# Kernel tuning notes

Measured on AMD Instinct MI355X. Metric: run time of the kernel, lower is better.

Reference implementation:

```python
import jax, jax.numpy as jnp
import numpy as np

B, N, D, H, DK, DV, HID = 4, 16384, 512, 8, 64, 64, 2048
LN_EPS = 1e-5   # torch nn.LayerNorm default
ATTN_EPS = 1e-6 # eps passed to LinearMultiHeadAttention


def _ln(h, g, b):
    m = jnp.mean(h, axis=-1, keepdims=True)
    v = jnp.mean(jnp.square(h - m), axis=-1, keepdims=True)
    return (h - m) * jax.lax.rsqrt(v + LN_EPS) * g + b


def setup_inputs() -> dict:
    key = jax.random.key(0)
    ks = jax.random.split(key, 8)
    w = lambda k, *sh: (jax.random.normal(k, sh, jnp.float32) * 0.02)
    return {
        "x": jax.random.normal(ks[0], (B, N, D), jnp.float32),
        "ln1_g": jnp.ones((D,), jnp.float32), "ln1_b": jnp.zeros((D,), jnp.float32),
        "Wq": w(ks[1], D, H * DK), "bq": jnp.zeros((H * DK,), jnp.float32),
        "Wk": w(ks[2], D, H * DK), "bk": jnp.zeros((H * DK,), jnp.float32),
        "Wv": w(ks[3], D, H * DV), "bv": jnp.zeros((H * DV,), jnp.float32),
        "Wo": w(ks[4], H * DV, D), "bo": jnp.zeros((D,), jnp.float32),
        "ln2_g": jnp.ones((D,), jnp.float32), "ln2_b": jnp.zeros((D,), jnp.float32),
        "W1": w(ks[5], D, HID), "b1": jnp.zeros((HID,), jnp.float32),
        "W2": w(ks[6], HID, D), "b2": jnp.zeros((D,), jnp.float32),
    }


def reference(x, ln1_g, ln1_b, Wq, bq, Wk, bk, Wv, bv, Wo, bo,
              ln2_g, ln2_b, W1, b1, W2, b2):
    # pre-LN (zero-width label concat is a no-op in label_embedded mode)
    h = _ln(x, ln1_g, ln1_b)                         # [B,N,D]
    q = (h @ Wq + bq).reshape(B, N, H, DK)
    k = (h @ Wk + bk).reshape(B, N, H, DK)
    v = (h @ Wv + bv).reshape(B, N, H, DV)
    # linear attention: phi = elu + 1 feature map, O(N) non-causal form
    pq = jax.nn.elu(q) + 1.0
    pk = jax.nn.elu(k) + 1.0
    kv = jnp.einsum('bnhd,bnhm->bhdm', pk, v)        # [B,H,DK,DV]
    ksum = jnp.sum(pk, axis=1)                       # [B,H,DK]
    z = 1.0 / (jnp.einsum('bnhd,bhd->bnh', pq, ksum) + ATTN_EPS)
    attn = jnp.einsum('bnhd,bhdm->bnhm', pq, kv) * z[..., None]
    attn = attn.reshape(B, N, H * DV) @ Wo + bo      # output projection
    h = h + attn                                     # residual 1
    h2 = _ln(h, ln2_g, ln2_b)
    dense = jax.nn.gelu(h2 @ W1 + b1) @ W2 + b2      # MLP, gelu activation
    return h2 + dense                                # residual 2
```

## Files before the change

kernel.cpp:

```cpp
#include <hip/hip_runtime.h>
#include <stdint.h>

#define BB   4
#define NN   16384
#define HH   8
#define DD   512
#define HIDN 2048
#define ROWST (BB * NN)

using short8 = __attribute__((ext_vector_type(8))) short;
using f32x4  = __attribute__((ext_vector_type(4))) float;

__device__ __forceinline__ float bf2f(uint16_t h) {
  union { uint32_t u; float f; } v; v.u = ((uint32_t)h) << 16; return v.f;
}
__device__ __forceinline__ uint16_t f2bf(float f) {
  union { float f; uint32_t u; } v; v.f = f;
  return (uint16_t)((v.u + 0x7FFFu + ((v.u >> 16) & 1u)) >> 16);
}
__device__ __forceinline__ float gelu_f(float x) {
  const float t1 = x * x;
  const float inner = __builtin_fmaf(0.044715f * t1, x, x);
  const float e = __expf(-1.5957691216f * inner);
  return x * __builtin_amdgcn_rcpf(1.f + e);
}
__device__ __forceinline__ void cp16(const uint16_t* g, uint16_t* l) {
  __builtin_amdgcn_global_load_lds((const __attribute__((address_space(1))) void*)g,
                                   (__attribute__((address_space(3))) void*)l, 16, 0, 0);
}
__device__ __forceinline__ int swz(int row, int col) {
  return row * 64 + (col ^ (row & 56));
}

template <int E>
__launch_bounds__(512, 2)
__global__ void gemm256(const uint16_t* __restrict__ A, const uint16_t* __restrict__ BT,
                        const float* __restrict__ bias, const uint16_t* __restrict__ res,
                        void* __restrict__ outp, int M, int N, int K) {
  __shared__ __align__(16) uint16_t S[65536];
  const int tid = threadIdx.x;
  const int lane = tid & 63, wave = tid >> 6;
  const int l15 = lane & 15, l4 = lane >> 4;
  const int wm = (wave >> 2) * 128, wn = (wave & 3) * 64;

  const int gx = gridDim.x;
  const int nwg = gx * gridDim.y;
  const int orig = blockIdx.y * gx + blockIdx.x;
  const int cpx = nwg >> 3;
  const int tile = (orig & 7) * cpx + (orig >> 3);
  const int tn = tile % gx, tm = tile / gx;
  const int m0 = tm * 256, n0 = tn * 256;

  const int bsw = (tid & 7) ^ ((tid >> 3) & 7);
  const int row_lo = ((tid >> 3) << 1) + (bsw >> 2);
  const int c8 = (bsw & 3) * 8;
  const uint16_t* pA = A  + (size_t)(m0 + row_lo) * K + c8;
  const uint16_t* pB = BT + (size_t)(n0 + row_lo) * K + c8;
  const size_t rstep = (size_t)128 * K;
  const int dstw = wave * 512;

  const int pbF = (((l15 & 1) << 2) | l4) ^ (l15 >> 1);
  const uint32_t sbase = (uint32_t)(uintptr_t)(__attribute__((address_space(3))) void*)S;
  const uint32_t aoff = sbase + (uint32_t)((wm * 32 + (l15 >> 1) * 64 + pbF * 8) * 2);
  const uint32_t boff = sbase + (uint32_t)((16384 + wn * 32 + (l15 >> 1) * 64 + pbF * 8) * 2);
  const uint32_t aB0_ = aoff,          aB1_ = aoff + 65536;
  const uint32_t bB0_ = boff,          bB1_ = boff + 65536;

  auto stageA = [&](int buf, int kh, int kb) {
    uint16_t* d = S + buf * 32768 + kh * 8192 + dstw;
    const uint16_t* s = pA + kb + kh * 32;
    cp16(s, d);
    cp16(s + rstep, d + 4096);
  };
  auto stageB = [&](int buf, int kh, int kb) {
    uint16_t* d = S + buf * 32768 + 16384 + kh * 8192 + dstw;
    const uint16_t* s = pB + kb + kh * 32;
    cp16(s, d);
    cp16(s + rstep, d + 4096);
  };

  f32x4 acc[8][4];
#pragma unroll
  for (int i = 0; i < 8; ++i)
#pragma unroll
    for (int j = 0; j < 4; ++j) acc[i][j] = (f32x4){0.f, 0.f, 0.f, 0.f};
  short8 bf[4];

  const int NT = K >> 6;
  stageA(0, 0, 0);  stageB(0, 0, 0);
  stageA(0, 1, 0);  stageB(0, 1, 0);
  stageA(1, 0, 64); stageB(1, 0, 64);
  __builtin_amdgcn_sched_barrier(0);
  asm volatile("s_waitcnt vmcnt(4)");
  __builtin_amdgcn_sched_barrier(0);
  __builtin_amdgcn_s_barrier();

#define DSR(dst, base, OFF)                                                      \
  asm volatile("ds_read_b128 %0, %1 offset:%2" : "=v"(dst) : "v"(base), "i"(OFF))

#define PHASE(BUF, MH, KH, RB, PRE, POST)                                        \
  {                                                                              \
    short8 af[4];                                                                \
    DSR(af[0], ((BUF) ? aB1_ : aB0_), (KH)*16384 + (MH)*4096 + 0*1024);          \
    DSR(af[1], ((BUF) ? aB1_ : aB0_), (KH)*16384 + (MH)*4096 + 1*1024);          \
    DSR(af[2], ((BUF) ? aB1_ : aB0_), (KH)*16384 + (MH)*4096 + 2*1024);          \
    DSR(af[3], ((BUF) ? aB1_ : aB0_), (KH)*16384 + (MH)*4096 + 3*1024);          \
    if (RB) {                                                                    \
      DSR(bf[0], ((BUF) ? bB1_ : bB0_), (KH)*16384 + 0*1024);                    \
      DSR(bf[1], ((BUF) ? bB1_ : bB0_), (KH)*16384 + 1*1024);                    \
      DSR(bf[2], ((BUF) ? bB1_ : bB0_), (KH)*16384 + 2*1024);                    \
      DSR(bf[3], ((BUF) ? bB1_ : bB0_), (KH)*16384 + 3*1024);                    \
    }                                                                            \
    PRE;                                                                         \
    __builtin_amdgcn_sched_barrier(0);                                           \
    __builtin_amdgcn_s_barrier();                                                \
    asm volatile("s_waitcnt lgkmcnt(0)");                                        \
    __builtin_amdgcn_sched_barrier(0);                                           \
    __builtin_amdgcn_s_setprio(1);                                               \
    _Pragma("unroll")                                                            \
    for (int i = 0; i < 4; ++i)                                                  \
      _Pragma("unroll")                                                          \
      for (int j = 0; j < 4; ++j)                                                \
        acc[(MH)*4 + i][j] = __builtin_amdgcn_mfma_f32_16x16x32_bf16(af[i], bf[j], acc[(MH)*4 + i][j], 0, 0, 0); \
    __builtin_amdgcn_s_setprio(0);                                               \
    __builtin_amdgcn_sched_barrier(0);                                           \
    POST;                                                                        \
    __builtin_amdgcn_sched_barrier(0);                                           \
    __builtin_amdgcn_s_barrier();                                                \
  }

  for (int t2 = 0; t2 < NT; t2 += 2) {
    {
      const int t = t2;
      const int kb1 = (t + 1) << 6, kb2 = (t + 2) << 6;
      PHASE(0, 0, 0, 1, if (t + 1 < NT) stageA(1, 1, kb1), {});
      PHASE(0, 1, 0, 0, if (t + 1 < NT) stageB(1, 1, kb1), {});
      PHASE(0, 0, 1, 1, if (t + 2 < NT) stageA(0, 0, kb2), {});
      PHASE(0, 1, 1, 0, if (t + 2 < NT) stageB(0, 0, kb2),
            if (t + 2 < NT) { asm volatile("s_waitcnt vmcnt(4)"); }
            else            { asm volatile("s_waitcnt vmcnt(0)"); });
    }
    {
      const int t = t2 + 1;
      const int kb1 = (t + 1) << 6, kb2 = (t + 2) << 6;
      PHASE(1, 0, 0, 1, if (t + 1 < NT) stageA(0, 1, kb1), {});
      PHASE(1, 1, 0, 0, if (t + 1 < NT) stageB(0, 1, kb1), {});
      PHASE(1, 0, 1, 1, if (t + 2 < NT) stageA(1, 0, kb2), {});
      PHASE(1, 1, 1, 0, if (t + 2 < NT) stageB(1, 0, kb2),
            if (t + 2 < NT) { asm volatile("s_waitcnt vmcnt(4)"); }
            else            { asm volatile("s_waitcnt vmcnt(0)"); });
    }
  }
#undef PHASE
#undef DSR

  __syncthreads();
  const float bj[4] = {bias[n0 + wn + l15], bias[n0 + wn + 16 + l15],
                       bias[n0 + wn + 32 + l15], bias[n0 + wn + 48 + l15]};
#pragma unroll
  for (int mf = 0; mf < 8; ++mf)
#pragma unroll
    for (int rg = 0; rg < 4; ++rg) {
      const int lrow = wm + mf * 16 + l4 * 4 + rg;
#pragma unroll
      for (int j = 0; j < 4; ++j) {
        const int lcol = wn + j * 16 + l15;
        float v = acc[mf][j][rg] + bj[j];
        if (E == 5) {
          if (n0 + lcol < 1024) v = v > 0.f ? v + 1.f : __expf(v);
        } else if (E == 3) {
          v = gelu_f(v);
        }
        S[lrow * 256 + ((((lcol >> 3) ^ lrow) & 31) * 8) + (lcol & 7)] = f2bf(v);
      }
    }
  __syncthreads();

  uint16_t* outb = (uint16_t*)outp;
  float* outf = (float*)outp;
  const int rr = tid >> 5;
  const int cb = tid & 31;
#pragma unroll
  for (int p = 0; p < 16; ++p) {
    const int lrow = p * 16 + rr;
    const int row = m0 + lrow;
    const int col0 = n0 + cb * 8;
    const uint4 d = *(const uint4*)&S[lrow * 256 + ((cb ^ lrow) & 31) * 8];
    if (E == 5) {
      const size_t offs = (size_t)(col0 >> 9) * ((size_t)ROWST * DD) +
                          (size_t)row * DD + (col0 & 511);
      *(uint4*)&outb[offs] = d;
    } else if (E == 1 || E == 3) {
      *(uint4*)&outb[(size_t)row * N + col0] = d;
    } else {
      const size_t idx = (size_t)row * N + col0;
      const uint4 rd = *(const uint4*)&res[idx];
      float a[8];
      a[0] = bf2f((uint16_t)(d.x & 0xffff)) + bf2f((uint16_t)(rd.x & 0xffff));
      a[1] = bf2f((uint16_t)(d.x >> 16))    + bf2f((uint16_t)(rd.x >> 16));
      a[2] = bf2f((uint16_t)(d.y & 0xffff)) + bf2f((uint16_t)(rd.y & 0xffff));
      a[3] = bf2f((uint16_t)(d.y >> 16))    + bf2f((uint16_t)(rd.y >> 16));
      a[4] = bf2f((uint16_t)(d.z & 0xffff)) + bf2f((uint16_t)(rd.z & 0xffff));
      a[5] = bf2f((uint16_t)(d.z >> 16))    + bf2f((uint16_t)(rd.z >> 16));
      a[6] = bf2f((uint16_t)(d.w & 0xffff)) + bf2f((uint16_t)(rd.w & 0xffff));
      a[7] = bf2f((uint16_t)(d.w >> 16))    + bf2f((uint16_t)(rd.w >> 16));
      if (E == 2) {
        uint4 o;
        o.x = (uint32_t)f2bf(a[0]) | ((uint32_t)f2bf(a[1]) << 16);
        o.y = (uint32_t)f2bf(a[2]) | ((uint32_t)f2bf(a[3]) << 16);
        o.z = (uint32_t)f2bf(a[4]) | ((uint32_t)f2bf(a[5]) << 16);
        o.w = (uint32_t)f2bf(a[6]) | ((uint32_t)f2bf(a[7]) << 16);
        *(uint4*)&outb[idx] = o;
      } else {
        *(float4*)&outf[idx]     = (float4){a[0], a[1], a[2], a[3]};
        *(float4*)&outf[idx + 4] = (float4){a[4], a[5], a[6], a[7]};
      }
    }
  }
}

template <int BFIN>
__launch_bounds__(256)
__global__ void ln_kernel(const void* __restrict__ inp, const float* __restrict__ gam,
                          const float* __restrict__ bet, uint16_t* __restrict__ out) {
  const int row = blockIdx.x * 4 + (threadIdx.x >> 6);
  const int lane = threadIdx.x & 63;
  const size_t base = (size_t)row * DD + lane * 8;
  float x[8];
  if (BFIN) {
    const uint4 u = *(const uint4*)((const uint16_t*)inp + base);
    x[0] = bf2f((uint16_t)(u.x & 0xffff)); x[1] = bf2f((uint16_t)(u.x >> 16));
    x[2] = bf2f((uint16_t)(u.y & 0xffff)); x[3] = bf2f((uint16_t)(u.y >> 16));
    x[4] = bf2f((uint16_t)(u.z & 0xffff)); x[5] = bf2f((uint16_t)(u.z >> 16));
    x[6] = bf2f((uint16_t)(u.w & 0xffff)); x[7] = bf2f((uint16_t)(u.w >> 16));
  } else {
    const float* f = (const float*)inp + base;
    const float4 a = *(const float4*)f;
    const float4 b = *(const float4*)(f + 4);
    x[0]=a.x; x[1]=a.y; x[2]=a.z; x[3]=a.w; x[4]=b.x; x[5]=b.y; x[6]=b.z; x[7]=b.w;
  }
  float s = 0.f, s2 = 0.f;
#pragma unroll
  for (int j = 0; j < 8; ++j) { s += x[j]; s2 += x[j] * x[j]; }
#pragma unroll
  for (int off = 32; off; off >>= 1) { s += __shfl_xor(s, off, 64); s2 += __shfl_xor(s2, off, 64); }
  const float m = s * (1.f / DD);
  const float rs = rsqrtf(s2 * (1.f / DD) - m * m + 1e-5f);
  uint16_t o[8];
#pragma unroll
  for (int j = 0; j < 8; ++j) {
    const int col = lane * 8 + j;
    o[j] = f2bf((x[j] - m) * rs * gam[col] + bet[col]);
  }
  uint4 w;
  w.x = (uint32_t)o[0] | ((uint32_t)o[1] << 16);
  w.y = (uint32_t)o[2] | ((uint32_t)o[3] << 16);
  w.z = (uint32_t)o[4] | ((uint32_t)o[5] << 16);
  w.w = (uint32_t)o[6] | ((uint32_t)o[7] << 16);
  *(uint4*)(out + base) = w;
}

__launch_bounds__(256)
__global__ void transpose_bf(const float* __restrict__ in, uint16_t* __restrict__ out,
                             int R, int C) {
  __shared__ float tile[32][33];
  const int tx = threadIdx.x, ty = threadIdx.y;
  const int c0 = blockIdx.x * 32, r0 = blockIdx.y * 32;
#pragma unroll
  for (int i = 0; i < 32; i += 8)
    tile[ty + i][tx] = in[(size_t)(r0 + ty + i) * C + (c0 + tx)];
  __syncthreads();
#pragma unroll
  for (int i = 0; i < 32; i += 8)
    out[(size_t)(c0 + ty + i) * R + (r0 + tx)] = f2bf(tile[tx][ty + i]);
}

__global__ void concat_bias(const float* __restrict__ bq, const float* __restrict__ bk,
                            const float* __restrict__ bv, float* __restrict__ o) {
  const int t = blockIdx.x * 256 + threadIdx.x;
  if (t < 512) o[t] = bq[t];
  else if (t < 1024) o[t] = bk[t - 512];
  else if (t < 1536) o[t] = bv[t - 1024];
}

__launch_bounds__(256)
__global__ void kv_mfma(const uint16_t* __restrict__ pk, const uint16_t* __restrict__ v,
                        float* __restrict__ kvp, float* __restrict__ ksp) {
  __shared__ __align__(16) uint16_t sT[4][2][64 * 64];
  __shared__ float ksred[64];
  const int bh = blockIdx.x, b = bh >> 3, h = bh & 7;
  const int t = threadIdx.x, lane = t & 63, w = t >> 6;
  const int l15 = lane & 15, l4 = lane >> 4;
  if (t < 64) ksred[t] = 0.f;
  __syncthreads();

  f32x4 acc[4][4];
#pragma unroll
  for (int i = 0; i < 4; ++i)
#pragma unroll
    for (int j = 0; j < 4; ++j) acc[i][j] = (f32x4){0.f, 0.f, 0.f, 0.f};
  float ks[4] = {0.f, 0.f, 0.f, 0.f};

  const int rl = lane >> 3, cl = (lane & 7) * 8;
  for (int sc = 0; sc < 4; ++sc) {
    const int nbase = blockIdx.y * 1024 + w * 256 + sc * 64;
#pragma unroll
    for (int ro = 0; ro < 8; ++ro) {
      const int n = ro * 8 + rl;
      const size_t gofs = ((size_t)(b * NN + nbase + n) * HH + h) * 64 + cl;
      const short8 pv = *(const short8*)(pk + gofs);
      const short8 vv = *(const short8*)(v + gofs);
#pragma unroll
      for (int j = 0; j < 8; ++j) {
        sT[w][0][swz(cl + j, n)] = (uint16_t)pv[j];
        sT[w][1][swz(cl + j, n)] = (uint16_t)vv[j];
      }
    }
#pragma unroll
    for (int kk = 0; kk < 64; kk += 32) {
      short8 af[4], bfr[4];
#pragma unroll
      for (int i = 0; i < 4; ++i)
        af[i] = *(const short8*)&sT[w][0][swz(i * 16 + l15, kk + l4 * 8)];
#pragma unroll
      for (int j = 0; j < 4; ++j)
        bfr[j] = *(const short8*)&sT[w][1][swz(j * 16 + l15, kk + l4 * 8)];
#pragma unroll
      for (int i = 0; i < 4; ++i) {
#pragma unroll
        for (int e = 0; e < 8; ++e) ks[i] += bf2f((uint16_t)af[i][e]);
#pragma unroll
        for (int j = 0; j < 4; ++j)
          acc[i][j] = __builtin_amdgcn_mfma_f32_16x16x32_bf16(af[i], bfr[j], acc[i][j], 0, 0, 0);
      }
    }
  }
#pragma unroll
  for (int i = 0; i < 4; ++i) {
    float s = ks[i];
    s += __shfl_xor(s, 16, 64); s += __shfl_xor(s, 32, 64);
    if (l4 == 0) atomicAdd(&ksred[i * 16 + l15], s);
  }
  __syncthreads();
  float* red = (float*)&sT[0][0][0];
  if (w > 0) {
#pragma unroll
    for (int i = 0; i < 4; ++i)
#pragma unroll
      for (int r = 0; r < 4; ++r)
#pragma unroll
        for (int j = 0; j < 4; ++j)
          red[(w - 1) * 4096 + (i * 16 + l4 * 4 + r) * 64 + j * 16 + l15] = acc[i][j][r];
  }
  __syncthreads();
  if (w == 0) {
    float* dst = kvp + ((size_t)bh * 16 + blockIdx.y) * 4096;
#pragma unroll
    for (int i = 0; i < 4; ++i)
#pragma unroll
      for (int r = 0; r < 4; ++r)
#pragma unroll
        for (int j = 0; j < 4; ++j) {
          const int e = (i * 16 + l4 * 4 + r) * 64 + j * 16 + l15;
          dst[e] = acc[i][j][r] + red[e] + red[4096 + e] + red[8192 + e];
        }
  }
  if (t < 64) ksp[((size_t)bh * 16 + blockIdx.y) * 64 + t] = ksred[t];
}

__launch_bounds__(256)
__global__ void kv_reduce(const float* __restrict__ kvp, const float* __restrict__ ksp,
                          float* __restrict__ kv, float* __restrict__ ksum) {
  const int bh = blockIdx.x;
  if (blockIdx.y == 16) {
    if (threadIdx.x < 64) {
      float s = 0.f;
      for (int c = 0; c < 16; ++c) s += ksp[((size_t)bh * 16 + c) * 64 + threadIdx.x];
      ksum[bh * 64 + threadIdx.x] = s;
    }
    return;
  }
  const int e = blockIdx.y * 256 + threadIdx.x;
  float s = 0.f;
  for (int c = 0; c < 16; ++c) s += kvp[((size_t)bh * 16 + c) * 4096 + e];
  kv[(size_t)bh * 4096 + e] = s;
}

__launch_bounds__(256)
__global__ void attn_mfma(const uint16_t* __restrict__ pq, const float* __restrict__ kv,
                          const float* __restrict__ ksum, uint16_t* __restrict__ attn) {
  __shared__ __align__(16) uint16_t kvT[64 * 64];
  __shared__ float ksS[64];
  __shared__ float denS[4][64];
  const int bh = blockIdx.x, b = bh >> 3, h = bh & 7;
  const int t = threadIdx.x, lane = t & 63, w = t >> 6;
  const int l15 = lane & 15, l4 = lane >> 4;
  const float* kvb = kv + (size_t)bh * 4096;
#pragma unroll
  for (int u = 0; u < 16; ++u) {
    const int e = u * 256 + t;
    kvT[swz(e & 63, e >> 6)] = f2bf(kvb[e]);
  }
  if (t < 64) ksS[t] = ksum[bh * 64 + t];
  __syncthreads();

  float ksr[16];
#pragma unroll
  for (int kk2 = 0; kk2 < 2; ++kk2) {
    const float4 k0 = *(const float4*)&ksS[kk2 * 32 + l4 * 8];
    const float4 k1 = *(const float4*)&ksS[kk2 * 32 + l4 * 8 + 4];
    ksr[kk2 * 8 + 0] = k0.x; ksr[kk2 * 8 + 1] = k0.y; ksr[kk2 * 8 + 2] = k0.z; ksr[kk2 * 8 + 3] = k0.w;
    ksr[kk2 * 8 + 4] = k1.x; ksr[kk2 * 8 + 5] = k1.y; ksr[kk2 * 8 + 6] = k1.z; ksr[kk2 * 8 + 7] = k1.w;
  }
  short8 bfrg[2][4];
#pragma unroll
  for (int kk2 = 0; kk2 < 2; ++kk2)
#pragma unroll
    for (int j = 0; j < 4; ++j)
      bfrg[kk2][j] = *(const short8*)&kvT[swz(j * 16 + l15, kk2 * 32 + l4 * 8)];

  const int n0w = blockIdx.y * 256 + w * 64;
  f32x4 acc[4][4];
#pragma unroll
  for (int i = 0; i < 4; ++i)
#pragma unroll
    for (int j = 0; j < 4; ++j) acc[i][j] = (f32x4){0.f, 0.f, 0.f, 0.f};
  float den[4] = {0.f, 0.f, 0.f, 0.f};

#pragma unroll
  for (int i = 0; i < 4; ++i) {
    const int n = n0w + i * 16 + l15;
    const size_t abase = ((size_t)(b * NN + n) * HH + h) * 64 + l4 * 8;
#pragma unroll
    for (int kk2 = 0; kk2 < 2; ++kk2) {
      const short8 af = *(const short8*)(pq + abase + kk2 * 32);
#pragma unroll
      for (int e = 0; e < 8; ++e) den[i] += bf2f((uint16_t)af[e]) * ksr[kk2 * 8 + e];
#pragma unroll
      for (int j = 0; j < 4; ++j)
        acc[i][j] = __builtin_amdgcn_mfma_f32_16x16x32_bf16(af, bfrg[kk2][j], acc[i][j], 0, 0, 0);
    }
  }
#pragma unroll
  for (int i = 0; i < 4; ++i) {
    float s = den[i];
    s += __shfl_xor(s, 16, 64); s += __shfl_xor(s, 32, 64);
    if (l4 == 0) denS[w][i * 16 + l15] = s;
  }
#pragma unroll
  for (int i = 0; i < 4; ++i)
#pragma unroll
    for (int r = 0; r < 4; ++r) {
      const float z = 1.f / (denS[w][i * 16 + l4 * 4 + r] + 1e-6f);
      const int n = n0w + i * 16 + l4 * 4 + r;
      const size_t ob = ((size_t)(b * NN + n) * HH + h) * 64;
#pragma unroll
      for (int j = 0; j < 4; ++j)
        attn[ob + j * 16 + l15] = f2bf(acc[i][j][r] * z);
    }
}

extern "C" void kernel_launch(void* const* d_in, const int* in_sizes, int n_in,
                              void* d_out, int out_size, void* d_ws, size_t ws_size,
                              hipStream_t stream) {
  (void)in_sizes; (void)n_in; (void)out_size;
  const float* x    = (const float*)d_in[0];
  const float* ln1g = (const float*)d_in[1];
  const float* ln1b = (const float*)d_in[2];
  const float* Wq   = (const float*)d_in[3];
  const float* bq   = (const float*)d_in[4];
  const float* Wk   = (const float*)d_in[5];
  const float* bk   = (const float*)d_in[6];
  const float* Wv   = (const float*)d_in[7];
  const float* bv   = (const float*)d_in[8];
  const float* Wo   = (const float*)d_in[9];
  const float* bo   = (const float*)d_in[10];
  const float* ln2g = (const float*)d_in[11];
  const float* ln2b = (const float*)d_in[12];
  const float* W1   = (const float*)d_in[13];
  const float* b1   = (const float*)d_in[14];
  const float* W2   = (const float*)d_in[15];
  const float* b2   = (const float*)d_in[16];

  if (ws_size < 409000000ULL) return;

  char* p = (char*)d_ws;
  auto alloc = [&](size_t bytes) -> char* {
    char* r = p; p += (bytes + 255) & ~(size_t)255; return r;
  };
  uint16_t* Hb  = (uint16_t*)alloc((size_t)ROWST * DD * 2);
  uint16_t* PQ  = (uint16_t*)alloc((size_t)ROWST * DD * 2);
  uint16_t* PK  = (uint16_t*)alloc((size_t)ROWST * DD * 2);
  uint16_t* PV  = (uint16_t*)alloc((size_t)ROWST * DD * 2);
  uint16_t* U   = (uint16_t*)alloc((size_t)32768 * HIDN * 2);
  uint16_t* WqkvT = (uint16_t*)alloc((size_t)1536 * DD * 2);
  uint16_t* WoT = (uint16_t*)alloc((size_t)DD * DD * 2);
  uint16_t* W1T = (uint16_t*)alloc((size_t)HIDN * DD * 2);
  uint16_t* W2T = (uint16_t*)alloc((size_t)DD * HIDN * 2);
  float*    bqkv = (float*)alloc(1536 * 4);
  float* KVP = (float*)U;
  float* KSP = KVP + 512 * 4096;
  float* KV  = KSP + 512 * 64;
  float* KS  = KV + 32 * 4096;

  const dim3 tb(32, 8);
  transpose_bf<<<dim3(16, 16), tb, 0, stream>>>(Wq, WqkvT, DD, DD);
  transpose_bf<<<dim3(16, 16), tb, 0, stream>>>(Wk, WqkvT + 512 * 512, DD, DD);
  transpose_bf<<<dim3(16, 16), tb, 0, stream>>>(Wv, WqkvT + 2 * 512 * 512, DD, DD);
  transpose_bf<<<dim3(16, 16), tb, 0, stream>>>(Wo, WoT, DD, DD);
  transpose_bf<<<dim3(64, 16), tb, 0, stream>>>(W1, W1T, DD, HIDN);
  transpose_bf<<<dim3(16, 64), tb, 0, stream>>>(W2, W2T, HIDN, DD);
  concat_bias<<<6, 256, 0, stream>>>(bq, bk, bv, bqkv);

  ln_kernel<0><<<ROWST / 4, 256, 0, stream>>>(x, ln1g, ln1b, Hb);
  gemm256<5><<<dim3(6, 256), 512, 0, stream>>>(Hb, WqkvT, bqkv, nullptr, PQ, ROWST, 1536, DD);
  kv_mfma<<<dim3(32, 16), 256, 0, stream>>>(PK, PV, KVP, KSP);
  kv_reduce<<<dim3(32, 17), 256, 0, stream>>>(KVP, KSP, KV, KS);
  attn_mfma<<<dim3(32, 64), 256, 0, stream>>>(PQ, KV, KS, PV);
  gemm256<2><<<dim3(2, 256), 512, 0, stream>>>(PV, WoT, bo, Hb, PK, ROWST, DD, DD);
  ln_kernel<1><<<ROWST / 4, 256, 0, stream>>>(PK, ln2g, ln2b, PQ);
  for (int c = 0; c < 2; ++c) {
    const uint16_t* h2c = PQ + (size_t)c * 32768 * DD;
    gemm256<3><<<dim3(8, 128), 512, 0, stream>>>(h2c, W1T, b1, nullptr, U, 32768, HIDN, DD);
    gemm256<4><<<dim3(2, 128), 512, 0, stream>>>(U, W2T, b2, h2c,
        (float*)d_out + (size_t)c * 32768 * DD, 32768, DD, HIDN);
  }
}
```

Before: 957.3 us.

## Merge GEMM phases per k-half with split LDS waits and smaller MLP chunks

The GEMM main loop now does two phases per k-tile instead of four. Each phase loads all eight A fragments and the four B fragments at once, then uses lgkmcnt(4) so the first half of the MFMAs can start while the second-half A reads are still in flight. This halves the number of workgroup barriers per tile and stages A and B together, at the cost of more live VGPRs (twelve fragments). Separately, the MLP is processed in four chunks of 16384 rows instead of two, which shrinks the U intermediate so it may stay in cache better, but launches more, smaller kernels.

Result: slower. 1.164 ms (+21.6%).

```diff
diff --git a/kernel.cpp b/kernel.cpp
--- a/kernel.cpp
+++ b/kernel.cpp
@@ -84,7 +84,6 @@
   for (int i = 0; i < 8; ++i)
 #pragma unroll
     for (int j = 0; j < 4; ++j) acc[i][j] = (f32x4){0.f, 0.f, 0.f, 0.f};
-  short8 bf[4];
 
   const int NT = K >> 6;
   stageA(0, 0, 0);  stageB(0, 0, 0);
@@ -98,60 +97,71 @@
 #define DSR(dst, base, OFF)                                                      \
   asm volatile("ds_read_b128 %0, %1 offset:%2" : "=v"(dst) : "v"(base), "i"(OFF))
 
-#define PHASE(BUF, MH, KH, RB, PRE, POST)                                        \
-  {                                                                              \
-    short8 af[4];                                                                \
-    DSR(af[0], ((BUF) ? aB1_ : aB0_), (KH)*16384 + (MH)*4096 + 0*1024);          \
-    DSR(af[1], ((BUF) ? aB1_ : aB0_), (KH)*16384 + (MH)*4096 + 1*1024);          \
-    DSR(af[2], ((BUF) ? aB1_ : aB0_), (KH)*16384 + (MH)*4096 + 2*1024);          \
-    DSR(af[3], ((BUF) ? aB1_ : aB0_), (KH)*16384 + (MH)*4096 + 3*1024);          \
-    if (RB) {                                                                    \
-      DSR(bf[0], ((BUF) ? bB1_ : bB0_), (KH)*16384 + 0*1024);                    \
-      DSR(bf[1], ((BUF) ? bB1_ : bB0_), (KH)*16384 + 1*1024);                    \
-      DSR(bf[2], ((BUF) ? bB1_ : bB0_), (KH)*16384 + 2*1024);                    \
-      DSR(bf[3], ((BUF) ? bB1_ : bB0_), (KH)*16384 + 3*1024);                    \
-    }                                                                            \
-    PRE;                                                                         \
-    __builtin_amdgcn_sched_barrier(0);                                           \
-    __builtin_amdgcn_s_barrier();                                                \
-    asm volatile("s_waitcnt lgkmcnt(0)");                                        \
-    __builtin_amdgcn_sched_barrier(0);                                           \
-    __builtin_amdgcn_s_setprio(1);                                               \
-    _Pragma("unroll")                                                            \
-    for (int i = 0; i < 4; ++i)                                                  \
-      _Pragma("unroll")                                                          \
-      for (int j = 0; j < 4; ++j)                                                \
-        acc[(MH)*4 + i][j] = __builtin_amdgcn_mfma_f32_16x16x32_bf16(af[i], bf[j], acc[(MH)*4 + i][j], 0, 0, 0); \
-    __builtin_amdgcn_s_setprio(0);                                               \
-    __builtin_amdgcn_sched_barrier(0);                                           \
-    POST;                                                                        \
-    __builtin_amdgcn_sched_barrier(0);                                           \
-    __builtin_amdgcn_s_barrier();                                                \
+#define SPHASE(BUF, KH, PRE, POST)                                              \
+  {                                                                             \
+    short8 af[8], bfr[4];                                                       \
+    DSR(af[0], ((BUF) ? aB1_ : aB0_), (KH)*16384 + 0*1024);                     \
+    DSR(af[1], ((BUF) ? aB1_ : aB0_), (KH)*16384 + 1*1024);                     \
+    DSR(af[2], ((BUF) ? aB1_ : aB0_), (KH)*16384 + 2*1024);                     \
+    DSR(af[3], ((BUF) ? aB1_ : aB0_), (KH)*16384 + 3*1024);                     \
+    DSR(bfr[0], ((BUF) ? bB1_ : bB0_), (KH)*16384 + 0*1024);                    \
+    DSR(bfr[1], ((BUF) ? bB1_ : bB0_), (KH)*16384 + 1*1024);                    \
+    DSR(bfr[2], ((BUF) ? bB1_ : bB0_), (KH)*16384 + 2*1024);                    \
+    DSR(bfr[3], ((BUF) ? bB1_ : bB0_), (KH)*16384 + 3*1024);                    \
+    DSR(af[4], ((BUF) ? aB1_ : aB0_), (KH)*16384 + 4096 + 0*1024);              \
+    DSR(af[5], ((BUF) ? aB1_ : aB0_), (KH)*16384 + 4096 + 1*1024);              \
+    DSR(af[6], ((BUF) ? aB1_ : aB0_), (KH)*16384 + 4096 + 2*1024);              \
+    DSR(af[7], ((BUF) ? aB1_ : aB0_), (KH)*16384 + 4096 + 3*1024);              \
+    PRE;                                                                        \
+    __builtin_amdgcn_sched_barrier(0);                                          \
+    asm volatile("s_waitcnt lgkmcnt(4)");                                       \
+    __builtin_amdgcn_sched_barrier(0);                                          \
+    __builtin_amdgcn_s_setprio(1);                                              \
+    _Pragma("unroll")                                                           \
+    for (int i = 0; i < 4; ++i)                                                 \
+      _Pragma("unroll")                                                         \
+      for (int j = 0; j < 4; ++j)                                               \
+        acc[i][j] = __builtin_amdgcn_mfma_f32_16x16x32_bf16(af[i], bfr[j], acc[i][j], 0, 0, 0); \
+    __builtin_amdgcn_s_setprio(0);                                              \
+    __builtin_amdgcn_sched_barrier(0);                                          \
+    asm volatile("s_waitcnt lgkmcnt(0)");                                       \
+    __builtin_amdgcn_sched_barrier(0);                                          \
+    __builtin_amdgcn_s_setprio(1);                                              \
+    _Pragma("unroll")                                                           \
+    for (int i = 0; i < 4; ++i)                                                 \
+      _Pragma("unroll")                                                         \
+      for (int j = 0; j < 4; ++j)                                               \
+        acc[4 + i][j] = __builtin_amdgcn_mfma_f32_16x16x32_bf16(af[4 + i], bfr[j], acc[4 + i][j], 0, 0, 0); \
+    __builtin_amdgcn_s_setprio(0);                                              \
+    __builtin_amdgcn_sched_barrier(0);                                          \
+    POST;                                                                       \
+    __builtin_amdgcn_sched_barrier(0);                                          \
+    __builtin_amdgcn_s_barrier();                                               \
   }
 
   for (int t2 = 0; t2 < NT; t2 += 2) {
     {
       const int t = t2;
       const int kb1 = (t + 1) << 6, kb2 = (t + 2) << 6;
-      PHASE(0, 0, 0, 1, if (t + 1 < NT) stageA(1, 1, kb1), {});
-      PHASE(0, 1, 0, 0, if (t + 1 < NT) stageB(1, 1, kb1), {});
-      PHASE(0, 0, 1, 1, if (t + 2 < NT) stageA(0, 0, kb2), {});
-      PHASE(0, 1, 1, 0, if (t + 2 < NT) stageB(0, 0, kb2),
-            if (t + 2 < NT) { asm volatile("s_waitcnt vmcnt(4)"); }
-            else            { asm volatile("s_waitcnt vmcnt(0)"); });
+      SPHASE(0, 0,
+             { if (t + 1 < NT) { stageA(1, 1, kb1); stageB(1, 1, kb1); } }, {});
+      SPHASE(0, 1,
+             { if (t + 2 < NT) { stageA(0, 0, kb2); stageB(0, 0, kb2); } },
+             { if (t + 2 < NT) { asm volatile("s_waitcnt vmcnt(4)"); }
+               else            { asm volatile("s_waitcnt vmcnt(0)"); } });
     }
     {
       const int t = t2 + 1;
       const int kb1 = (t + 1) << 6, kb2 = (t + 2) << 6;
-      PHASE(1, 0, 0, 1, if (t + 1 < NT) stageA(0, 1, kb1), {});
-      PHASE(1, 1, 0, 0, if (t + 1 < NT) stageB(0, 1, kb1), {});
-      PHASE(1, 0, 1, 1, if (t + 2 < NT) stageA(1, 0, kb2), {});
-      PHASE(1, 1, 1, 0, if (t + 2 < NT) stageB(1, 0, kb2),
-            if (t + 2 < NT) { asm volatile("s_waitcnt vmcnt(4)"); }
-            else            { asm volatile("s_waitcnt vmcnt(0)"); });
-    }
-  }
-#undef PHASE
+      SPHASE(1, 0,
+             { if (t + 1 < NT) { stageA(0, 1, kb1); stageB(0, 1, kb1); } }, {});
+      SPHASE(1, 1,
+             { if (t + 2 < NT) { stageA(1, 0, kb2); stageB(1, 0, kb2); } },
+             { if (t + 2 < NT) { asm volatile("s_waitcnt vmcnt(4)"); }
+               else            { asm volatile("s_waitcnt vmcnt(0)"); } });
+    }
+  }
+#undef SPHASE
 #undef DSR
 
   __syncthreads();
@@ -519,10 +529,10 @@
   attn_mfma<<<dim3(32, 64), 256, 0, stream>>>(PQ, KV, KS, PV);
   gemm256<2><<<dim3(2, 256), 512, 0, stream>>>(PV, WoT, bo, Hb, PK, ROWST, DD, DD);
   ln_kernel<1><<<ROWST / 4, 256, 0, stream>>>(PK, ln2g, ln2b, PQ);
-  for (int c = 0; c < 2; ++c) {
-    const uint16_t* h2c = PQ + (size_t)c * 32768 * DD;
-    gemm256<3><<<dim3(8, 128), 512, 0, stream>>>(h2c, W1T, b1, nullptr, U, 32768, HIDN, DD);
-    gemm256<4><<<dim3(2, 128), 512, 0, stream>>>(U, W2T, b2, h2c,
-        (float*)d_out + (size_t)c * 32768 * DD, 32768, DD, HIDN);
-  }
-}
+  for (int c = 0; c < 4; ++c) {
+    const uint16_t* h2c = PQ + (size_t)c * 16384 * DD;
+    gemm256<3><<<dim3(8, 64), 512, 0, stream>>>(h2c, W1T, b1, nullptr, U, 16384, HIDN, DD);
+    gemm256<4><<<dim3(2, 64), 512, 0, stream>>>(U, W2T, b2, h2c,
+        (float*)d_out + (size_t)c * 16384 * DD, 16384, DD, HIDN);
+  }
+}
```
